# Kernel optimization log

Measured on AMD Instinct MI355X. Metric: run time of the kernel, lower is better.

## Reference

```python
import jax, jax.numpy as jnp
import numpy as np

SEQ_LEN = 2048
N_FFT = 4096  # nearest power of two >= 2*SEQ_LEN - 1
K = 24
D_IN = 512
D_OUT = 512
K_U = 3


def setup_inputs() -> dict:
    key = jax.random.key(0)
    k1, k2, k3, k4, k5 = jax.random.split(key, 5)
    x = jax.random.normal(k1, (1, SEQ_LEN, D_IN), dtype=jnp.float32)
    phi = jax.random.normal(k2, (SEQ_LEN, K), dtype=jnp.float32)
    M = jax.random.normal(k3, (D_OUT, D_IN, K_U), dtype=jnp.float32) / D_IN
    M_phi_plus = jax.random.normal(k4, (K, D_IN, D_OUT), dtype=jnp.float32) / 10.0
    M_phi_minus = jax.random.normal(k5, (K, D_IN, D_OUT), dtype=jnp.float32) / 10.0
    return {"x": x, "phi": phi, "M": M, "M_phi_plus": M_phi_plus, "M_phi_minus": M_phi_minus}


def _convolve(u, v, n):
    # u: (bsz, seq, d_in); v: (seq, K) spectral filters
    bsz, seq_len, d_in = u.shape
    Kf = v.shape[1]
    # alternating sign (+1, -1, +1, ...) along time, shape (1, seq, 1, 1)
    sgn = jnp.where(jnp.arange(seq_len) % 2 == 1, -1.0, 1.0).reshape(1, seq_len, 1, 1)
    v_f = jnp.fft.rfft(v.astype(jnp.float32).reshape(1, seq_len, Kf, 1, 1), n=n, axis=1)
    u_exp = jnp.broadcast_to(u[:, :, None, :], (bsz, seq_len, Kf, d_in))
    # stack [u, u*sgn] -> (bsz, seq, K, d_in, 2)
    U = jnp.stack([u_exp, u_exp * sgn], axis=-1).astype(jnp.float32)
    U_f = jnp.fft.rfft(U, n=n, axis=1)
    U_conv = jnp.fft.irfft(v_f * U_f, n=n, axis=1)[:, :seq_len]
    U_plus = U_conv[..., 0]
    U_minus = U_conv[..., 1] * sgn  # (b, seq, K, d_in) * (1, seq, 1, 1)
    return U_plus, U_minus


def _ar_preds(M, x):
    # M: (d_out, d_in, k_u); x: (b, l, d_in)
    # ar[t] = sum_{i=0}^{k_u-1} M[:,:,i] @ x[t-i]  (zero before start)
    b, l, _ = x.shape
    out = jnp.zeros((b, l, M.shape[0]), dtype=x.dtype)
    for i in range(M.shape[-1]):
        x_shift = jnp.pad(x, ((0, 0), (i, 0), (0, 0)))[:, :l]
        out = out + jnp.einsum("bli,oi->blo", x_shift, M[:, :, i])
    return out


def reference(x, phi, M, M_phi_plus, M_phi_minus):
    U_plus, U_minus = _convolve(x, phi, N_FFT)
    spectral_plus = jnp.einsum("blkd,kdo->blo", U_plus, M_phi_plus)
    spectral_minus = jnp.einsum("blkd,kdo->blo", U_minus, M_phi_minus)
    output = spectral_plus + spectral_minus  # use_hankel_L=False
    ar = _ar_preds(M, x)
    return output + ar
```

## Files before the change

kernel.cpp:

```cpp
#include <hip/hip_runtime.h>

typedef __bf16 bf16;
typedef bf16 bf16x8 __attribute__((ext_vector_type(8)));
typedef float floatx16 __attribute__((ext_vector_type(16)));

#define AS1 __attribute__((address_space(1)))
#define AS3 __attribute__((address_space(3)))

#define KTOT 26112

__device__ __forceinline__ void stage_tile(const bf16* g, int ld, bf16* lds, int tid) {
#pragma unroll
    for (int it = 0; it < 4; ++it) {
        int q    = it * 256 + tid;
        int row  = q >> 3;
        int col8 = (q & 7) ^ (row & 7);
        __builtin_amdgcn_global_load_lds(
            (const AS1 void*)(g + (size_t)row * ld + col8 * 8),
            (AS3 void*)(lds + q * 8), 16, 0, 0);
    }
}

__device__ __forceinline__ void mfma_block(const bf16* lA, const bf16* lB,
                                           floatx16 acc[2][2], int lane, int wm, int wn) {
    const int lrow = lane & 31;
    const int lk   = lane >> 5;
#pragma unroll
    for (int s = 0; s < 4; ++s) {
        bf16x8 af[2], bfr[2];
        const int c8 = s * 2 + lk;
#pragma unroll
        for (int mi = 0; mi < 2; ++mi) {
            int r = wm * 64 + mi * 32 + lrow;
            af[mi] = *(const bf16x8*)(lA + r * 64 + ((c8 ^ (r & 7)) << 3));
        }
#pragma unroll
        for (int ni = 0; ni < 2; ++ni) {
            int r = wn * 64 + ni * 32 + lrow;
            bfr[ni] = *(const bf16x8*)(lB + r * 64 + ((c8 ^ (r & 7)) << 3));
        }
#pragma unroll
        for (int mi = 0; mi < 2; ++mi)
#pragma unroll
            for (int ni = 0; ni < 2; ++ni)
                acc[mi][ni] = __builtin_amdgcn_mfma_f32_32x32x16_bf16(
                    af[mi], bfr[ni], acc[mi][ni], 0, 0, 0);
    }
}

#define CD_ROW(r, lane) (((r) & 3) + 8 * ((r) >> 2) + 4 * ((lane) >> 5))

__global__ __launch_bounds__(256) void conv_gemm(const bf16* __restrict__ Tb,
                                                 const bf16* __restrict__ xT2,
                                                 bf16* __restrict__ A2) {
    __shared__ bf16 lA[128 * 64], lB[128 * 64];
    const int tid = threadIdx.x;
    const int lane = tid & 63, wave = tid >> 6, wm = wave & 1, wn = wave >> 1;
    const int bid = blockIdx.x;
    const int a    = 7 - (bid / 384);
    const int rem  = bid % 384;
    const int dblk = rem / 48;
    const int kw   = rem % 48;

    floatx16 acc[2][2];
#pragma unroll
    for (int mi = 0; mi < 2; ++mi)
#pragma unroll
        for (int ni = 0; ni < 2; ++ni)
#pragma unroll
            for (int e = 0; e < 16; ++e) acc[mi][ni][e] = 0.f;

    for (int c = 0; c <= a; ++c) {
        const bf16* Ab = Tb + ((size_t)kw * 8 + (a - c)) * 16384;
        const bf16* Bb = xT2 + (size_t)(dblk * 128) * 1024 + c * 128;
#pragma unroll
        for (int kk = 0; kk < 128; kk += 64) {
            stage_tile(Ab + kk, 128, lA, tid);
            stage_tile(Bb + kk, 1024, lB, tid);
            __syncthreads();
            mfma_block(lA, lB, acc, lane, wm, wn);
            __syncthreads();
        }
    }
    const int w = kw & 1, k = kw >> 1;
    const int kv = w ? (24 + k) : k;
    const int p = dblk >> 2, dbase = (dblk & 3) * 128;
    bf16* Ocol = A2 + (size_t)kv * 512 + dbase;
#pragma unroll
    for (int mi = 0; mi < 2; ++mi)
#pragma unroll
        for (int ni = 0; ni < 2; ++ni)
#pragma unroll
            for (int r = 0; r < 16; ++r) {
                int tau = a * 128 + wm * 64 + mi * 32 + CD_ROW(r, lane);
                int t = 2 * tau + p + w;
                if (t < 2048) {
                    int col = wn * 64 + ni * 32 + (lane & 31);
                    Ocol[(size_t)t * KTOT + col] = (bf16)acc[mi][ni][r];
                }
            }
}

__global__ __launch_bounds__(256) void proj_gemm(const bf16* __restrict__ A2,
                                                 const bf16* __restrict__ B2,
                                                 float* __restrict__ P2) {
    __shared__ bf16 lA[2][128 * 64], lB[2][128 * 64];
    const int tid = threadIdx.x;
    const int lane = tid & 63, wave = tid >> 6, wm = wave & 1, wn = wave >> 1;
    const int bm = blockIdx.x, sp = blockIdx.y, bn = blockIdx.z;
    const bf16* Ab = A2 + (size_t)bm * 128 * KTOT + sp * 3264;
    const bf16* Bb = B2 + (size_t)bn * 128 * KTOT + sp * 3264;

    floatx16 acc[2][2];
#pragma unroll
    for (int mi = 0; mi < 2; ++mi)
#pragma unroll
        for (int ni = 0; ni < 2; ++ni)
#pragma unroll
            for (int e = 0; e < 16; ++e) acc[mi][ni][e] = 0.f;

    stage_tile(Ab, KTOT, lA[0], tid);
    stage_tile(Bb, KTOT, lB[0], tid);
    __syncthreads();
    int cur = 0;
    for (int kk = 0; kk < 3264; kk += 64) {
        if (kk + 64 < 3264) {
            stage_tile(Ab + kk + 64, KTOT, lA[cur ^ 1], tid);
            stage_tile(Bb + kk + 64, KTOT, lB[cur ^ 1], tid);
        }
        mfma_block(lA[cur], lB[cur], acc, lane, wm, wn);
        __syncthreads();
        cur ^= 1;
    }
    float* Pt = P2 + (size_t)sp * 1048576;
#pragma unroll
    for (int mi = 0; mi < 2; ++mi)
#pragma unroll
        for (int ni = 0; ni < 2; ++ni)
#pragma unroll
            for (int r = 0; r < 16; ++r) {
                int t = bm * 128 + wm * 64 + mi * 32 + CD_ROW(r, lane);
                int o = bn * 128 + wn * 64 + ni * 32 + (lane & 31);
                Pt[(size_t)t * 512 + o] = acc[mi][ni][r];
            }
}

__global__ void prep_all(const float* __restrict__ x, const float* __restrict__ phi,
                         const float* __restrict__ M, const float* __restrict__ Mp,
                         const float* __restrict__ Mm, bf16* __restrict__ xT2,
                         bf16* __restrict__ A2, bf16* __restrict__ B2,
                         bf16* __restrict__ Tb) {
    __shared__ float smem[2][64 * 65];
    const int b = blockIdx.x, tid = threadIdx.x;
    if (b < 256) {
        int dpt = (b >> 4) * 64, st = (b & 15) * 64;
        int p = dpt >> 9, dbase = dpt & 511;
#pragma unroll
        for (int it = 0; it < 16; ++it) {
            int q = it * 256 + tid;
            int r = q >> 6, cc = q & 63;
            smem[0][r * 65 + cc] = x[(size_t)(2 * (st + r) + p) * 512 + dbase + cc];
        }
        __syncthreads();
#pragma unroll
        for (int it = 0; it < 2; ++it) {
            int q = it * 256 + tid;
            int r = q >> 3, c8 = q & 7;
            bf16x8 v;
#pragma unroll
            for (int jj = 0; jj < 8; ++jj)
                v[jj] = (bf16)smem[0][(c8 * 8 + jj) * 65 + r];
            *(bf16x8*)&xT2[(size_t)(dpt + r) * 1024 + st + c8 * 8] = v;
        }
    } else if (b < 1792) {
        int idx8 = (b - 256) * 256 + tid;
        int t = idx8 / 192, q = idx8 % 192;
        int i = q >> 6, d8 = (q & 63) * 8;
        bf16x8 v;
        if (t - i >= 0) {
            const float* xp = x + (size_t)(t - i) * 512 + d8;
            float4 f0 = *(const float4*)(xp);
            float4 f1 = *(const float4*)(xp + 4);
            v[0] = (bf16)f0.x; v[1] = (bf16)f0.y; v[2] = (bf16)f0.z; v[3] = (bf16)f0.w;
            v[4] = (bf16)f1.x; v[5] = (bf16)f1.y; v[6] = (bf16)f1.z; v[7] = (bf16)f1.w;
        } else {
#pragma unroll
            for (int jj = 0; jj < 8; ++jj) v[jj] = (bf16)0.f;
        }
        *(bf16x8*)(A2 + (size_t)t * KTOT + 24576 + i * 512 + d8) = v;
    } else if (b < 3328) {
        int b2 = b - 1792;
        int k = b2 >> 6, rem2 = b2 & 63;
        int dt = (rem2 >> 3) * 64, ot = (rem2 & 7) * 64;
        const float* Sp = Mp + (size_t)k * 262144;
        const float* Sm = Mm + (size_t)k * 262144;
#pragma unroll
        for (int it = 0; it < 16; ++it) {
            int q = it * 256 + tid;
            int r = q >> 6, cc = q & 63;
            smem[0][r * 65 + cc] = Sp[(size_t)(dt + r) * 512 + ot + cc];
            smem[1][r * 65 + cc] = Sm[(size_t)(dt + r) * 512 + ot + cc];
        }
        __syncthreads();
#pragma unroll
        for (int it = 0; it < 2; ++it) {
            int q = it * 256 + tid;
            int r = q >> 3, c8 = q & 7;
            bf16x8 vs, vd;
#pragma unroll
            for (int jj = 0; jj < 8; ++jj) {
                float av = smem[0][(c8 * 8 + jj) * 65 + r];
                float bv = smem[1][(c8 * 8 + jj) * 65 + r];
                vs[jj] = (bf16)(av + bv);
                vd[jj] = (bf16)(av - bv);
            }
            *(bf16x8*)&B2[(size_t)(ot + r) * KTOT + k * 512 + dt + c8 * 8] = vs;
            *(bf16x8*)&B2[(size_t)(ot + r) * KTOT + (24 + k) * 512 + dt + c8 * 8] = vd;
        }
    } else if (b < 3840) {
        int o = b - 3328;
        for (int q = tid; q < 1536; q += 256) smem[0][q] = M[(size_t)o * 1536 + q];
        __syncthreads();
        if (tid < 192) {
            int q = tid * 8;
            int i = q >> 9, d0 = q & 511;
            bf16x8 v;
#pragma unroll
            for (int jj = 0; jj < 8; ++jj) v[jj] = (bf16)smem[0][(d0 + jj) * 3 + i];
            *(bf16x8*)&B2[(size_t)o * KTOT + 24576 + q] = v;
        }
    } else if (b < 4224) {
        int b3 = b - 3840;
        int kw = b3 >> 3, m = b3 & 7;
        int k = kw >> 1, w = kw & 1;
        if (tid < 255) {
            int sh = m * 128 - 127 + tid;
            smem[0][tid] = (sh >= 0) ? phi[(size_t)(2 * sh + w) * 24 + k] : 0.f;
        }
        __syncthreads();
        bf16* Tp = Tb + (size_t)b3 * 16384;
#pragma unroll
        for (int it = 0; it < 8; ++it) {
            int q = it * 256 + tid;
            int i = q >> 4, j8 = (q & 15) * 8;
            bf16x8 v;
#pragma unroll
            for (int jj = 0; jj < 8; ++jj)
                v[jj] = (bf16)smem[0][127 + i - (j8 + jj)];
            *(bf16x8*)(Tp + i * 128 + j8) = v;
        }
    } else {
        int off = 12288 + (b - 4224) * 2048 + tid * 8;
        bf16x8 z;
#pragma unroll
        for (int jj = 0; jj < 8; ++jj) z[jj] = (bf16)0.f;
        *(bf16x8*)(A2 + off) = z;
    }
}

__global__ void reduce8(const float* __restrict__ P2, float* __restrict__ out) {
    int idx = blockIdx.x * 256 + threadIdx.x;
    if (idx >= 2048 * 512) return;
    float s = 0.f;
#pragma unroll
    for (int sp = 0; sp < 8; ++sp)
        s += P2[(size_t)sp * 1048576 + idx];
    out[idx] = s;
}

extern "C" void kernel_launch(void* const* d_in, const int* in_sizes, int n_in,
                              void* d_out, int out_size, void* d_ws, size_t ws_size,
                              hipStream_t stream) {
    const float* x   = (const float*)d_in[0];
    const float* phi = (const float*)d_in[1];
    const float* M   = (const float*)d_in[2];
    const float* Mp  = (const float*)d_in[3];
    const float* Mm  = (const float*)d_in[4];
    float* out = (float*)d_out;
    char* ws = (char*)d_ws;

    bf16*  Tb  = (bf16*)(ws + 0);
    bf16*  xT2 = (bf16*)(ws + 12582912);
    bf16*  A2  = (bf16*)(ws + 14680064);
    bf16*  B2  = (bf16*)(ws + 121634816);
    float* P2  = (float*)(ws + 148373504);

    prep_all<<<4230, 256, 0, stream>>>(x, phi, M, Mp, Mm, xT2, A2, B2, Tb);
    conv_gemm<<<3072, 256, 0, stream>>>(Tb, xT2, A2);
    proj_gemm<<<dim3(16, 8, 4), 256, 0, stream>>>(A2, B2, P2);
    reduce8<<<4096, 256, 0, stream>>>(P2, out);
}
```

Baseline: 252.9 us.

## Store projection operands in contiguous 128x64 tiled blocks for GEMM staging

Changes the A2/B2 operand layout from row-major with a 26112-element leading dimension to tile-blocked storage, where each 128-row by 64-column chunk is contiguous (8192 elements). Every producer (Toeplitz conv output, AR shifted x, spectral weight and M packing, zero fill) now writes into this blocked layout. The projection GEMM then stages each tile from one contiguous 16KB region instead of 128 widely strided rows. The aim is better DRAM/TLB locality for the split-K GEMM loads. In exchange, the scattered writes in the producers get more complex, and the zero-fill indexing must still cover the same region correctly.

```diff
diff --git a/kernel.cpp b/kernel.cpp
--- a/kernel.cpp
+++ b/kernel.cpp
@@ -7,7 +7,7 @@
 #define AS1 __attribute__((address_space(1)))
 #define AS3 __attribute__((address_space(3)))
 
-#define KTOT 26112
+#define NKB 408
 
 __device__ __forceinline__ void stage_tile(const bf16* g, int ld, bf16* lds, int tid) {
 #pragma unroll
@@ -84,8 +84,8 @@
     }
     const int w = kw & 1, k = kw >> 1;
     const int kv = w ? (24 + k) : k;
-    const int p = dblk >> 2, dbase = (dblk & 3) * 128;
-    bf16* Ocol = A2 + (size_t)kv * 512 + dbase;
+    const int p = dblk >> 2;
+    const int kb = kv * 8 + (dblk & 3) * 2 + wn;
 #pragma unroll
     for (int mi = 0; mi < 2; ++mi)
 #pragma unroll
@@ -95,8 +95,8 @@
                 int tau = a * 128 + wm * 64 + mi * 32 + CD_ROW(r, lane);
                 int t = 2 * tau + p + w;
                 if (t < 2048) {
-                    int col = wn * 64 + ni * 32 + (lane & 31);
-                    Ocol[(size_t)t * KTOT + col] = (bf16)acc[mi][ni][r];
+                    A2[((size_t)(t >> 7) * NKB + kb) * 8192 + (t & 127) * 64
+                       + ni * 32 + (lane & 31)] = (bf16)acc[mi][ni][r];
                 }
             }
 }
@@ -108,8 +108,8 @@
     const int tid = threadIdx.x;
     const int lane = tid & 63, wave = tid >> 6, wm = wave & 1, wn = wave >> 1;
     const int bm = blockIdx.x, sp = blockIdx.y, bn = blockIdx.z;
-    const bf16* Ab = A2 + (size_t)bm * 128 * KTOT + sp * 3264;
-    const bf16* Bb = B2 + (size_t)bn * 128 * KTOT + sp * 3264;
+    const bf16* Abase = A2 + ((size_t)bm * NKB + sp * 51) * 8192;
+    const bf16* Bbase = B2 + ((size_t)bn * NKB + sp * 51) * 8192;
 
     floatx16 acc[2][2];
 #pragma unroll
@@ -119,14 +119,14 @@
 #pragma unroll
             for (int e = 0; e < 16; ++e) acc[mi][ni][e] = 0.f;
 
-    stage_tile(Ab, KTOT, lA[0], tid);
-    stage_tile(Bb, KTOT, lB[0], tid);
+    stage_tile(Abase, 64, lA[0], tid);
+    stage_tile(Bbase, 64, lB[0], tid);
     __syncthreads();
     int cur = 0;
-    for (int kk = 0; kk < 3264; kk += 64) {
-        if (kk + 64 < 3264) {
-            stage_tile(Ab + kk + 64, KTOT, lA[cur ^ 1], tid);
-            stage_tile(Bb + kk + 64, KTOT, lB[cur ^ 1], tid);
+    for (int ti = 0; ti < 51; ++ti) {
+        if (ti + 1 < 51) {
+            stage_tile(Abase + (size_t)(ti + 1) * 8192, 64, lA[cur ^ 1], tid);
+            stage_tile(Bbase + (size_t)(ti + 1) * 8192, 64, lB[cur ^ 1], tid);
         }
         mfma_block(lA[cur], lB[cur], acc, lane, wm, wn);
         __syncthreads();
@@ -187,7 +187,9 @@
 #pragma unroll
             for (int jj = 0; jj < 8; ++jj) v[jj] = (bf16)0.f;
         }
-        *(bf16x8*)(A2 + (size_t)t * KTOT + 24576 + i * 512 + d8) = v;
+        int kb = 384 + i * 8 + (d8 >> 6);
+        *(bf16x8*)(A2 + ((size_t)(t >> 7) * NKB + kb) * 8192
+                      + (t & 127) * 64 + (d8 & 63)) = v;
     } else if (b < 3328) {
         int b2 = b - 1792;
         int k = b2 >> 6, rem2 = b2 & 63;
@@ -202,6 +204,7 @@
             smem[1][r * 65 + cc] = Sm[(size_t)(dt + r) * 512 + ot + cc];
         }
         __syncthreads();
+        int kb = k * 8 + (rem2 >> 3);
 #pragma unroll
         for (int it = 0; it < 2; ++it) {
             int q = it * 256 + tid;
@@ -214,8 +217,11 @@
                 vs[jj] = (bf16)(av + bv);
                 vd[jj] = (bf16)(av - bv);
             }
-            *(bf16x8*)&B2[(size_t)(ot + r) * KTOT + k * 512 + dt + c8 * 8] = vs;
-            *(bf16x8*)&B2[(size_t)(ot + r) * KTOT + (24 + k) * 512 + dt + c8 * 8] = vd;
+            int o = ot + r;
+            size_t rowoff = (size_t)(o & 127) * 64 + c8 * 8;
+            size_t base = (size_t)(o >> 7) * NKB;
+            *(bf16x8*)&B2[(base + kb) * 8192 + rowoff]       = vs;
+            *(bf16x8*)&B2[(base + kb + 192) * 8192 + rowoff] = vd;
         }
     } else if (b < 3840) {
         int o = b - 3328;
@@ -227,7 +233,8 @@
             bf16x8 v;
 #pragma unroll
             for (int jj = 0; jj < 8; ++jj) v[jj] = (bf16)smem[0][(d0 + jj) * 3 + i];
-            *(bf16x8*)&B2[(size_t)o * KTOT + 24576 + q] = v;
+            *(bf16x8*)&B2[((size_t)(o >> 7) * NKB + 384 + (tid >> 3)) * 8192
+                          + (o & 127) * 64 + (tid & 7) * 8] = v;
         }
     } else if (b < 4224) {
         int b3 = b - 3840;
@@ -250,11 +257,12 @@
             *(bf16x8*)(Tp + i * 128 + j8) = v;
         }
     } else {
-        int off = 12288 + (b - 4224) * 2048 + tid * 8;
+        int idx = (b - 4224) * 2048 + tid * 8;
+        int kb = 192 + (idx >> 6), colk = idx & 63;
         bf16x8 z;
 #pragma unroll
         for (int jj = 0; jj < 8; ++jj) z[jj] = (bf16)0.f;
-        *(bf16x8*)(A2 + off) = z;
+        *(bf16x8*)(A2 + (size_t)kb * 8192 + colk) = z;
     }
 }
 
```

Result: slower. 262.0 us (+3.6%).

## Split prep kernel and overlap weight prep with conv GEMM launch

Applied to the files above, without the earlier changes.

The prep kernel is split in two. Only the x transpose and the Toeplitz filter build, which the conv GEMM depends on, stay in a small first kernel. The independent preparation work (AR shifted inputs, projection weight sum/difference transposes, M repacking, zero padding) moves into extra blocks appended to the conv GEMM launch, so it runs alongside the GEMM blocks and fills idle CUs in the tail. This trades a larger, heterogeneous grid and shared LDS sizing (the GEMM blocks now reserve the larger float buffer) for less serialized prep time.

```diff
diff --git a/kernel.cpp b/kernel.cpp
--- a/kernel.cpp
+++ b/kernel.cpp
@@ -50,107 +50,9 @@
 
 #define CD_ROW(r, lane) (((r) & 3) + 8 * ((r) >> 2) + 4 * ((lane) >> 5))
 
-__global__ __launch_bounds__(256) void conv_gemm(const bf16* __restrict__ Tb,
-                                                 const bf16* __restrict__ xT2,
-                                                 bf16* __restrict__ A2) {
-    __shared__ bf16 lA[128 * 64], lB[128 * 64];
-    const int tid = threadIdx.x;
-    const int lane = tid & 63, wave = tid >> 6, wm = wave & 1, wn = wave >> 1;
-    const int bid = blockIdx.x;
-    const int a    = 7 - (bid / 384);
-    const int rem  = bid % 384;
-    const int dblk = rem / 48;
-    const int kw   = rem % 48;
-
-    floatx16 acc[2][2];
-#pragma unroll
-    for (int mi = 0; mi < 2; ++mi)
-#pragma unroll
-        for (int ni = 0; ni < 2; ++ni)
-#pragma unroll
-            for (int e = 0; e < 16; ++e) acc[mi][ni][e] = 0.f;
-
-    for (int c = 0; c <= a; ++c) {
-        const bf16* Ab = Tb + ((size_t)kw * 8 + (a - c)) * 16384;
-        const bf16* Bb = xT2 + (size_t)(dblk * 128) * 1024 + c * 128;
-#pragma unroll
-        for (int kk = 0; kk < 128; kk += 64) {
-            stage_tile(Ab + kk, 128, lA, tid);
-            stage_tile(Bb + kk, 1024, lB, tid);
-            __syncthreads();
-            mfma_block(lA, lB, acc, lane, wm, wn);
-            __syncthreads();
-        }
-    }
-    const int w = kw & 1, k = kw >> 1;
-    const int kv = w ? (24 + k) : k;
-    const int p = dblk >> 2, dbase = (dblk & 3) * 128;
-    bf16* Ocol = A2 + (size_t)kv * 512 + dbase;
-#pragma unroll
-    for (int mi = 0; mi < 2; ++mi)
-#pragma unroll
-        for (int ni = 0; ni < 2; ++ni)
-#pragma unroll
-            for (int r = 0; r < 16; ++r) {
-                int tau = a * 128 + wm * 64 + mi * 32 + CD_ROW(r, lane);
-                int t = 2 * tau + p + w;
-                if (t < 2048) {
-                    int col = wn * 64 + ni * 32 + (lane & 31);
-                    Ocol[(size_t)t * KTOT + col] = (bf16)acc[mi][ni][r];
-                }
-            }
-}
-
-__global__ __launch_bounds__(256) void proj_gemm(const bf16* __restrict__ A2,
-                                                 const bf16* __restrict__ B2,
-                                                 float* __restrict__ P2) {
-    __shared__ bf16 lA[2][128 * 64], lB[2][128 * 64];
-    const int tid = threadIdx.x;
-    const int lane = tid & 63, wave = tid >> 6, wm = wave & 1, wn = wave >> 1;
-    const int bm = blockIdx.x, sp = blockIdx.y, bn = blockIdx.z;
-    const bf16* Ab = A2 + (size_t)bm * 128 * KTOT + sp * 3264;
-    const bf16* Bb = B2 + (size_t)bn * 128 * KTOT + sp * 3264;
-
-    floatx16 acc[2][2];
-#pragma unroll
-    for (int mi = 0; mi < 2; ++mi)
-#pragma unroll
-        for (int ni = 0; ni < 2; ++ni)
-#pragma unroll
-            for (int e = 0; e < 16; ++e) acc[mi][ni][e] = 0.f;
-
-    stage_tile(Ab, KTOT, lA[0], tid);
-    stage_tile(Bb, KTOT, lB[0], tid);
-    __syncthreads();
-    int cur = 0;
-    for (int kk = 0; kk < 3264; kk += 64) {
-        if (kk + 64 < 3264) {
-            stage_tile(Ab + kk + 64, KTOT, lA[cur ^ 1], tid);
-            stage_tile(Bb + kk + 64, KTOT, lB[cur ^ 1], tid);
-        }
-        mfma_block(lA[cur], lB[cur], acc, lane, wm, wn);
-        __syncthreads();
-        cur ^= 1;
-    }
-    float* Pt = P2 + (size_t)sp * 1048576;
-#pragma unroll
-    for (int mi = 0; mi < 2; ++mi)
-#pragma unroll
-        for (int ni = 0; ni < 2; ++ni)
-#pragma unroll
-            for (int r = 0; r < 16; ++r) {
-                int t = bm * 128 + wm * 64 + mi * 32 + CD_ROW(r, lane);
-                int o = bn * 128 + wn * 64 + ni * 32 + (lane & 31);
-                Pt[(size_t)t * 512 + o] = acc[mi][ni][r];
-            }
-}
-
-__global__ void prep_all(const float* __restrict__ x, const float* __restrict__ phi,
-                         const float* __restrict__ M, const float* __restrict__ Mp,
-                         const float* __restrict__ Mm, bf16* __restrict__ xT2,
-                         bf16* __restrict__ A2, bf16* __restrict__ B2,
-                         bf16* __restrict__ Tb) {
-    __shared__ float smem[2][64 * 65];
+__global__ void prep_io(const float* __restrict__ x, const float* __restrict__ phi,
+                        bf16* __restrict__ xT2, bf16* __restrict__ Tb) {
+    __shared__ float smem[64 * 65];
     const int b = blockIdx.x, tid = threadIdx.x;
     if (b < 256) {
         int dpt = (b >> 4) * 64, st = (b & 15) * 64;
@@ -159,7 +61,7 @@
         for (int it = 0; it < 16; ++it) {
             int q = it * 256 + tid;
             int r = q >> 6, cc = q & 63;
-            smem[0][r * 65 + cc] = x[(size_t)(2 * (st + r) + p) * 512 + dbase + cc];
+            smem[r * 65 + cc] = x[(size_t)(2 * (st + r) + p) * 512 + dbase + cc];
         }
         __syncthreads();
 #pragma unroll
@@ -169,11 +71,96 @@
             bf16x8 v;
 #pragma unroll
             for (int jj = 0; jj < 8; ++jj)
-                v[jj] = (bf16)smem[0][(c8 * 8 + jj) * 65 + r];
+                v[jj] = (bf16)smem[(c8 * 8 + jj) * 65 + r];
             *(bf16x8*)&xT2[(size_t)(dpt + r) * 1024 + st + c8 * 8] = v;
         }
-    } else if (b < 1792) {
-        int idx8 = (b - 256) * 256 + tid;
+    } else {
+        int b3 = b - 256;
+        int kw = b3 >> 3, m = b3 & 7;
+        int k = kw >> 1, w = kw & 1;
+        if (tid < 255) {
+            int sh = m * 128 - 127 + tid;
+            smem[tid] = (sh >= 0) ? phi[(size_t)(2 * sh + w) * 24 + k] : 0.f;
+        }
+        __syncthreads();
+        bf16* Tp = Tb + (size_t)b3 * 16384;
+#pragma unroll
+        for (int it = 0; it < 8; ++it) {
+            int q = it * 256 + tid;
+            int i = q >> 4, j8 = (q & 15) * 8;
+            bf16x8 v;
+#pragma unroll
+            for (int jj = 0; jj < 8; ++jj)
+                v[jj] = (bf16)smem[127 + i - (j8 + jj)];
+            *(bf16x8*)(Tp + i * 128 + j8) = v;
+        }
+    }
+}
+
+__global__ __launch_bounds__(256) void conv_plus(const bf16* __restrict__ Tb,
+                                                 const bf16* __restrict__ xT2,
+                                                 bf16* __restrict__ A2,
+                                                 const float* __restrict__ x,
+                                                 const float* __restrict__ M,
+                                                 const float* __restrict__ Mp,
+                                                 const float* __restrict__ Mm,
+                                                 bf16* __restrict__ B2) {
+    __shared__ float smemf[2][64 * 65];
+    const int tid = threadIdx.x;
+    const int bid = blockIdx.x;
+
+    if (bid < 3072) {
+        bf16* lA = (bf16*)smemf;
+        bf16* lB = lA + 128 * 64;
+        const int lane = tid & 63, wave = tid >> 6, wm = wave & 1, wn = wave >> 1;
+        const int a    = 7 - (bid / 384);
+        const int rem  = bid % 384;
+        const int dblk = rem / 48;
+        const int kw   = rem % 48;
+
+        floatx16 acc[2][2];
+#pragma unroll
+        for (int mi = 0; mi < 2; ++mi)
+#pragma unroll
+            for (int ni = 0; ni < 2; ++ni)
+#pragma unroll
+                for (int e = 0; e < 16; ++e) acc[mi][ni][e] = 0.f;
+
+        for (int c = 0; c <= a; ++c) {
+            const bf16* Ab = Tb + ((size_t)kw * 8 + (a - c)) * 16384;
+            const bf16* Bb = xT2 + (size_t)(dblk * 128) * 1024 + c * 128;
+#pragma unroll
+            for (int kk = 0; kk < 128; kk += 64) {
+                stage_tile(Ab + kk, 128, lA, tid);
+                stage_tile(Bb + kk, 1024, lB, tid);
+                __syncthreads();
+                mfma_block(lA, lB, acc, lane, wm, wn);
+                __syncthreads();
+            }
+        }
+        const int w = kw & 1, k = kw >> 1;
+        const int kv = w ? (24 + k) : k;
+        const int p = dblk >> 2, dbase = (dblk & 3) * 128;
+        bf16* Ocol = A2 + (size_t)kv * 512 + dbase;
+#pragma unroll
+        for (int mi = 0; mi < 2; ++mi)
+#pragma unroll
+            for (int ni = 0; ni < 2; ++ni)
+#pragma unroll
+                for (int r = 0; r < 16; ++r) {
+                    int tau = a * 128 + wm * 64 + mi * 32 + CD_ROW(r, lane);
+                    int t = 2 * tau + p + w;
+                    if (t < 2048) {
+                        int col = wn * 64 + ni * 32 + (lane & 31);
+                        Ocol[(size_t)t * KTOT + col] = (bf16)acc[mi][ni][r];
+                    }
+                }
+        return;
+    }
+
+    const int b = bid - 3072;
+    if (b < 1536) {
+        int idx8 = b * 256 + tid;
         int t = idx8 / 192, q = idx8 % 192;
         int i = q >> 6, d8 = (q & 63) * 8;
         bf16x8 v;
@@ -188,8 +175,8 @@
             for (int jj = 0; jj < 8; ++jj) v[jj] = (bf16)0.f;
         }
         *(bf16x8*)(A2 + (size_t)t * KTOT + 24576 + i * 512 + d8) = v;
-    } else if (b < 3328) {
-        int b2 = b - 1792;
+    } else if (b < 3072) {
+        int b2 = b - 1536;
         int k = b2 >> 6, rem2 = b2 & 63;
         int dt = (rem2 >> 3) * 64, ot = (rem2 & 7) * 64;
         const float* Sp = Mp + (size_t)k * 262144;
@@ -198,8 +185,8 @@
         for (int it = 0; it < 16; ++it) {
             int q = it * 256 + tid;
             int r = q >> 6, cc = q & 63;
-            smem[0][r * 65 + cc] = Sp[(size_t)(dt + r) * 512 + ot + cc];
-            smem[1][r * 65 + cc] = Sm[(size_t)(dt + r) * 512 + ot + cc];
+            smemf[0][r * 65 + cc] = Sp[(size_t)(dt + r) * 512 + ot + cc];
+            smemf[1][r * 65 + cc] = Sm[(size_t)(dt + r) * 512 + ot + cc];
         }
         __syncthreads();
 #pragma unroll
@@ -209,53 +196,78 @@
             bf16x8 vs, vd;
 #pragma unroll
             for (int jj = 0; jj < 8; ++jj) {
-                float av = smem[0][(c8 * 8 + jj) * 65 + r];
-                float bv = smem[1][(c8 * 8 + jj) * 65 + r];
+                float av = smemf[0][(c8 * 8 + jj) * 65 + r];
+                float bv = smemf[1][(c8 * 8 + jj) * 65 + r];
                 vs[jj] = (bf16)(av + bv);
                 vd[jj] = (bf16)(av - bv);
             }
             *(bf16x8*)&B2[(size_t)(ot + r) * KTOT + k * 512 + dt + c8 * 8] = vs;
             *(bf16x8*)&B2[(size_t)(ot + r) * KTOT + (24 + k) * 512 + dt + c8 * 8] = vd;
         }
-    } else if (b < 3840) {
-        int o = b - 3328;
-        for (int q = tid; q < 1536; q += 256) smem[0][q] = M[(size_t)o * 1536 + q];
+    } else if (b < 3584) {
+        int o = b - 3072;
+        float* sm = smemf[0];
+        for (int q = tid; q < 1536; q += 256) sm[q] = M[(size_t)o * 1536 + q];
         __syncthreads();
         if (tid < 192) {
             int q = tid * 8;
             int i = q >> 9, d0 = q & 511;
             bf16x8 v;
 #pragma unroll
-            for (int jj = 0; jj < 8; ++jj) v[jj] = (bf16)smem[0][(d0 + jj) * 3 + i];
+            for (int jj = 0; jj < 8; ++jj) v[jj] = (bf16)sm[(d0 + jj) * 3 + i];
             *(bf16x8*)&B2[(size_t)o * KTOT + 24576 + q] = v;
         }
-    } else if (b < 4224) {
-        int b3 = b - 3840;
-        int kw = b3 >> 3, m = b3 & 7;
-        int k = kw >> 1, w = kw & 1;
-        if (tid < 255) {
-            int sh = m * 128 - 127 + tid;
-            smem[0][tid] = (sh >= 0) ? phi[(size_t)(2 * sh + w) * 24 + k] : 0.f;
-        }
-        __syncthreads();
-        bf16* Tp = Tb + (size_t)b3 * 16384;
-#pragma unroll
-        for (int it = 0; it < 8; ++it) {
-            int q = it * 256 + tid;
-            int i = q >> 4, j8 = (q & 15) * 8;
-            bf16x8 v;
-#pragma unroll
-            for (int jj = 0; jj < 8; ++jj)
-                v[jj] = (bf16)smem[0][127 + i - (j8 + jj)];
-            *(bf16x8*)(Tp + i * 128 + j8) = v;
-        }
     } else {
-        int off = 12288 + (b - 4224) * 2048 + tid * 8;
+        int off = 12288 + (b - 3584) * 2048 + tid * 8;
         bf16x8 z;
 #pragma unroll
         for (int jj = 0; jj < 8; ++jj) z[jj] = (bf16)0.f;
         *(bf16x8*)(A2 + off) = z;
     }
+}
+
+__global__ __launch_bounds__(256) void proj_gemm(const bf16* __restrict__ A2,
+                                                 const bf16* __restrict__ B2,
+                                                 float* __restrict__ P2) {
+    __shared__ bf16 lA[2][128 * 64], lB[2][128 * 64];
+    const int tid = threadIdx.x;
+    const int lane = tid & 63, wave = tid >> 6, wm = wave & 1, wn = wave >> 1;
+    const int bm = blockIdx.x, sp = blockIdx.y, bn = blockIdx.z;
+    const bf16* Ab = A2 + (size_t)bm * 128 * KTOT + sp * 3264;
+    const bf16* Bb = B2 + (size_t)bn * 128 * KTOT + sp * 3264;
+
+    floatx16 acc[2][2];
+#pragma unroll
+    for (int mi = 0; mi < 2; ++mi)
+#pragma unroll
+        for (int ni = 0; ni < 2; ++ni)
+#pragma unroll
+            for (int e = 0; e < 16; ++e) acc[mi][ni][e] = 0.f;
+
+    stage_tile(Ab, KTOT, lA[0], tid);
+    stage_tile(Bb, KTOT, lB[0], tid);
+    __syncthreads();
+    int cur = 0;
+    for (int kk = 0; kk < 3264; kk += 64) {
+        if (kk + 64 < 3264) {
+            stage_tile(Ab + kk + 64, KTOT, lA[cur ^ 1], tid);
+            stage_tile(Bb + kk + 64, KTOT, lB[cur ^ 1], tid);
+        }
+        mfma_block(lA[cur], lB[cur], acc, lane, wm, wn);
+        __syncthreads();
+        cur ^= 1;
+    }
+    float* Pt = P2 + (size_t)sp * 1048576;
+#pragma unroll
+    for (int mi = 0; mi < 2; ++mi)
+#pragma unroll
+        for (int ni = 0; ni < 2; ++ni)
+#pragma unroll
+            for (int r = 0; r < 16; ++r) {
+                int t = bm * 128 + wm * 64 + mi * 32 + CD_ROW(r, lane);
+                int o = bn * 128 + wn * 64 + ni * 32 + (lane & 31);
+                Pt[(size_t)t * 512 + o] = acc[mi][ni][r];
+            }
 }
 
 __global__ void reduce8(const float* __restrict__ P2, float* __restrict__ out) {
@@ -285,8 +297,8 @@
     bf16*  B2  = (bf16*)(ws + 121634816);
     float* P2  = (float*)(ws + 148373504);
 
-    prep_all<<<4230, 256, 0, stream>>>(x, phi, M, Mp, Mm, xT2, A2, B2, Tb);
-    conv_gemm<<<3072, 256, 0, stream>>>(Tb, xT2, A2);
+    prep_io<<<640, 256, 0, stream>>>(x, phi, xT2, Tb);
+    conv_plus<<<6662, 256, 0, stream>>>(Tb, xT2, A2, x, M, Mp, Mm, B2);
     proj_gemm<<<dim3(16, 8, 4), 256, 0, stream>>>(A2, B2, P2);
     reduce8<<<4096, 256, 0, stream>>>(P2, out);
 }
```

Result: slower. 262.3 us (+3.7%).
